# Kernel tuning notes

Hardware: AMD Instinct MI355X
Metric: run time of the kernel (lower is better)

Reference implementation:

```python
import jax, jax.numpy as jnp
import numpy as np

B, S, SK = 4, 256, 512
D, NH, NKV, HD = 1024, 16, 4, 64
DE, NE = 4096, 8
LANG_CODES = jnp.arange(4, 4 + NE)  # expert language codes (codes > 3 are routed)
LN_EPS = 1e-5


def setup_inputs() -> dict:
    key = jax.random.key(0)
    ks = jax.random.split(key, 32)
    sc = 0.02
    n = lambda k, shape: jax.random.normal(k, shape, jnp.float32)
    causal = jnp.where(jnp.tril(jnp.ones((S, S), bool)), 0.0, -1e9).astype(jnp.float32)
    inp = {
        "hidden_states": n(ks[0], (B, S, D)),
        "encoder_hidden_states": n(ks[1], (B, SK, D)),
        "attention_mask": jnp.broadcast_to(causal, (B, 1, S, S)),
        "encoder_attention_mask": jnp.zeros((B, 1, S, SK), jnp.float32),
        "langs": jax.random.randint(ks[2], (B, 2), 0, 12),
        "ln1_g": jnp.ones((D,), jnp.float32), "ln1_b": jnp.zeros((D,), jnp.float32),
        "sa_q_w": n(ks[3], (D, D)) * sc, "sa_q_b": jnp.zeros((D,), jnp.float32),
        "sa_k_w": n(ks[4], (D, NKV * HD)) * sc, "sa_k_b": jnp.zeros((NKV * HD,), jnp.float32),
        "sa_v_w": n(ks[5], (D, NKV * HD)) * sc, "sa_v_b": jnp.zeros((NKV * HD,), jnp.float32),
        "sa_o_w": n(ks[6], (D, D)) * sc, "sa_o_b": jnp.zeros((D,), jnp.float32),
        "ln2_g": jnp.ones((D,), jnp.float32), "ln2_b": jnp.zeros((D,), jnp.float32),
        "ca_q_w": n(ks[7], (D, D)) * sc, "ca_q_b": jnp.zeros((D,), jnp.float32),
        "ca_k_w": n(ks[8], (D, NKV * HD)) * sc, "ca_k_b": jnp.zeros((NKV * HD,), jnp.float32),
        "ca_v_w": n(ks[9], (D, NKV * HD)) * sc, "ca_v_b": jnp.zeros((NKV * HD,), jnp.float32),
        "ca_o_w": n(ks[10], (D, D)) * sc, "ca_o_b": jnp.zeros((D,), jnp.float32),
        "ln3_g": jnp.ones((D,), jnp.float32), "ln3_b": jnp.zeros((D,), jnp.float32),
        "moe_w1": n(ks[11], (NE, D, DE)) * sc,
        "moe_w2": n(ks[12], (NE, DE, D)) * sc,
        "moe_w3": n(ks[13], (NE, D, DE)) * sc,
    }
    return inp


def _ln(x, g, b):
    m = jnp.mean(x, -1, keepdims=True)
    v = jnp.var(x, -1, keepdims=True)
    return (x - m) * jax.lax.rsqrt(v + LN_EPS) * g + b


def _gqa(x, kv, qw, qb, kw, kb, vw, vb, ow, ob, mask):
    b, sq, _ = x.shape
    skv = kv.shape[1]
    q = ((x @ qw + qb) * HD ** -0.5).reshape(b, sq, NH, HD)
    k = (kv @ kw + kb).reshape(b, skv, NKV, HD)
    v = (kv @ vw + vb).reshape(b, skv, NKV, HD)
    rep = NH // NKV
    k = jnp.repeat(k, rep, axis=2)  # head h = kv_head*rep + r, matches repeat_kv
    v = jnp.repeat(v, rep, axis=2)
    scores = jnp.einsum('bqhd,bkhd->bhqk', q, k) + mask
    p = jax.nn.softmax(scores, axis=-1)
    o = jnp.einsum('bhqk,bkhd->bqhd', p, v).reshape(b, sq, NH * HD)
    return o @ ow + ob


def _moe(x, w1, w2, w3, langs):
    # routing: weight 1/(# lang codes > 3) per sequence; 1 if none
    counts = jnp.sum(langs > 3, axis=-1)
    rw = jnp.where(counts == 0, 1.0, 1.0 / jnp.maximum(counts, 1).astype(x.dtype))  # [B]
    match = jnp.any(langs[None, :, :] == LANG_CODES[:, None, None], axis=-1)  # [E,B]
    coef = match.astype(x.dtype) * rw[None, :]  # [E,B]
    h = jax.nn.gelu(jnp.einsum('bsd,edf->ebsf', x, w1), approximate=False) \
        * jnp.einsum('bsd,edf->ebsf', x, w3)
    out = jnp.einsum('ebsf,efd->ebsd', h, w2)
    return jnp.einsum('ebsd,eb->bsd', out, coef)


def reference(hidden_states, encoder_hidden_states, attention_mask, encoder_attention_mask,
              langs, ln1_g, ln1_b, sa_q_w, sa_q_b, sa_k_w, sa_k_b, sa_v_w, sa_v_b,
              sa_o_w, sa_o_b, ln2_g, ln2_b, ca_q_w, ca_q_b, ca_k_w, ca_k_b, ca_v_w,
              ca_v_b, ca_o_w, ca_o_b, ln3_g, ln3_b, moe_w1, moe_w2, moe_w3):
    # self attention (causal GQA, prefill, pre-LN)
    r = hidden_states
    h = _ln(hidden_states, ln1_g, ln1_b)
    h = _gqa(h, h, sa_q_w, sa_q_b, sa_k_w, sa_k_b, sa_v_w, sa_v_b, sa_o_w, sa_o_b,
             attention_mask)
    h = r + h
    # cross attention over encoder states
    r = h
    h = _ln(h, ln2_g, ln2_b)
    h = _gqa(h, encoder_hidden_states, ca_q_w, ca_q_b, ca_k_w, ca_k_b, ca_v_w, ca_v_b,
             ca_o_w, ca_o_b, encoder_attention_mask)
    h = r + h
    # language-routed MoE FFN
    r = h
    h = _ln(h, ln3_g, ln3_b)
    h = _moe(h, moe_w1, moe_w2, moe_w3, langs)
    return r + h
```

## Files before the change

### kernel.cpp

```cpp
#include <hip/hip_runtime.h>
#include <math.h>

#define B_   4
#define S_   256
#define SK_  512
#define D_   1024
#define NH_  16
#define NKV_ 4
#define HD_  64
#define DE_  4096
#define NE_  8

typedef __attribute__((ext_vector_type(8))) short bf16x8;
typedef __attribute__((ext_vector_type(4))) float f32x4;

__device__ __forceinline__ unsigned short f2b(float f) {
  union { float f; unsigned u; } v; v.f = f;
  unsigned r = v.u + 0x7FFF + ((v.u >> 16) & 1);
  return (unsigned short)(r >> 16);
}


__device__ __forceinline__ void stage_A_f32(const float* __restrict__ A, int lda, int k0, short* As) {
  int tid = threadIdx.x;
  int am = tid >> 2, ak8 = (tid & 3) * 8;
  const float* ap = A + (size_t)am * lda + k0 + ak8;
  float4 a0 = *(const float4*)ap;
  float4 a1 = *(const float4*)(ap + 4);
  const float* f0 = (const float*)&a0;
  const float* f1 = (const float*)&a1;
  bf16x8 v;
  v[0]=f2b(f0[0]); v[1]=f2b(f0[1]); v[2]=f2b(f0[2]); v[3]=f2b(f0[3]);
  v[4]=f2b(f1[0]); v[5]=f2b(f1[1]); v[6]=f2b(f1[2]); v[7]=f2b(f1[3]);
  *(bf16x8*)(As + am * 40 + ak8) = v;
}

__device__ __forceinline__ void stage_A_bf16(const short* __restrict__ A, int lda, int k0, short* As) {
  int tid = threadIdx.x;
  int am = tid >> 2, ak8 = (tid & 3) * 8;
  *(bf16x8*)(As + am * 40 + ak8) = *(const bf16x8*)(A + (size_t)am * lda + k0 + ak8);
}

__device__ __forceinline__ void stage_W_f32(const float* __restrict__ W, int ldw, int k0, short* Ws) {
  int tid = threadIdx.x;
  int wk2 = (tid & 15) * 2, wn4 = (tid >> 4) * 4;
  const float* wp = W + (size_t)(k0 + wk2) * ldw + wn4;
  float4 w0 = *(const float4*)wp;
  float4 w1 = *(const float4*)(wp + ldw);
  const float* f0 = (const float*)&w0;
  const float* f1 = (const float*)&w1;
#pragma unroll
  for (int c = 0; c < 4; ++c) {
    unsigned p = (unsigned)f2b(f0[c]) | ((unsigned)f2b(f1[c]) << 16);
    *(unsigned*)(Ws + (wn4 + c) * 40 + wk2) = p;
  }
}

__device__ __forceinline__ void mfma_quad(const short* As, const short* Ws, f32x4 acc[2][2]) {
  int lane = threadIdx.x & 63, wv = threadIdx.x >> 6;
  int wm = (wv & 1) * 32, wn = (wv >> 1) * 32;
  int quad = lane >> 4, l16 = lane & 15;
  bf16x8 a0 = *(const bf16x8*)(As + (wm + l16) * 40 + quad * 8);
  bf16x8 a1 = *(const bf16x8*)(As + (wm + 16 + l16) * 40 + quad * 8);
  bf16x8 b0 = *(const bf16x8*)(Ws + (wn + l16) * 40 + quad * 8);
  bf16x8 b1 = *(const bf16x8*)(Ws + (wn + 16 + l16) * 40 + quad * 8);
  acc[0][0] = __builtin_amdgcn_mfma_f32_16x16x32_bf16(a0, b0, acc[0][0], 0, 0, 0);
  acc[0][1] = __builtin_amdgcn_mfma_f32_16x16x32_bf16(a0, b1, acc[0][1], 0, 0, 0);
  acc[1][0] = __builtin_amdgcn_mfma_f32_16x16x32_bf16(a1, b0, acc[1][0], 0, 0, 0);
  acc[1][1] = __builtin_amdgcn_mfma_f32_16x16x32_bf16(a1, b1, acc[1][1], 0, 0, 0);
}

__device__ __forceinline__ void gemm_body(const float* A, const float* W, const float* bias,
                                          const float* resid, float* C, float scale,
                                          int N, int K, int bm, int bn,
                                          short* As, short* Ws) {
  f32x4 z4 = {0.f, 0.f, 0.f, 0.f};
  f32x4 acc[2][2] = {{z4, z4}, {z4, z4}};
  const float* Ab = A + (size_t)bm * K;
  const float* Wb = W + bn;
  for (int k0 = 0; k0 < K; k0 += 32) {
    stage_A_f32(Ab, K, k0, As);
    stage_W_f32(Wb, N, k0, Ws);
    __syncthreads();
    mfma_quad(As, Ws, acc);
    __syncthreads();
  }
  int lane = threadIdx.x & 63, wv = threadIdx.x >> 6;
  int wm = (wv & 1) * 32, wn = (wv >> 1) * 32;
  int quad = lane >> 4, l16 = lane & 15;
#pragma unroll
  for (int i = 0; i < 2; ++i)
#pragma unroll
    for (int j = 0; j < 2; ++j)
#pragma unroll
      for (int r = 0; r < 4; ++r) {
        int m = bm + wm + i * 16 + quad * 4 + r;
        int n = bn + wn + j * 16 + l16;
        float v = (acc[i][j][r] + bias[n]) * scale;
        if (resid) v += resid[(size_t)m * N + n];
        C[(size_t)m * N + n] = v;
      }
}

__global__ __launch_bounds__(256) void qkv_mfma(const float* __restrict__ xq, const float* __restrict__ xkv,
                                                const float* qw, const float* qb,
                                                const float* kw, const float* kb,
                                                const float* vw, const float* vb,
                                                float* qo, float* ko, float* vo,
                                                int Mq, int Mkv) {
  int z = blockIdx.z;
  const float *A, *W, *bias; float* out; int M, N; float scale;
  if (z == 0)      { A = xq;  W = qw; bias = qb; out = qo; M = Mq;  N = D_;  scale = 0.125f; }
  else if (z == 1) { A = xkv; W = kw; bias = kb; out = ko; M = Mkv; N = 256; scale = 1.0f; }
  else             { A = xkv; W = vw; bias = vb; out = vo; M = Mkv; N = 256; scale = 1.0f; }
  int bn = blockIdx.x * 64, bm = blockIdx.y * 64;
  if (bm >= M || bn >= N) return;
  __shared__ short As[64 * 40], Ws[64 * 40];
  gemm_body(A, W, bias, nullptr, out, scale, N, D_, bm, bn, As, Ws);
}

__global__ __launch_bounds__(256) void gemm_mfma(const float* __restrict__ A, const float* __restrict__ W,
                                                 const float* __restrict__ bias,
                                                 const float* resid, float* C,
                                                 float scale, int N, int K) {
  int bn = blockIdx.x * 64, bm = blockIdx.y * 64;
  __shared__ short As[64 * 40], Ws[64 * 40];
  gemm_body(A, W, bias, resid, C, scale, N, K, bm, bn, As, Ws);
}

__global__ __launch_bounds__(256) void moe_gate_mfma(const float* __restrict__ xln,
                                                     const float* __restrict__ W1,
                                                     const float* __restrict__ W3,
                                                     short* __restrict__ Hs,
                                                     const float* __restrict__ coef,
                                                     const int* __restrict__ slot) {
  int e = blockIdx.z;
  int bn = blockIdx.x * 64, bm = blockIdx.y * 64;
  int b = bm >> 8;
  if (coef[e * B_ + b] == 0.0f) return;
  int sl = slot[e * B_ + b];
  __shared__ short As[64 * 40], W1s[64 * 40], W3s[64 * 40];
  f32x4 z4 = {0.f, 0.f, 0.f, 0.f};
  f32x4 acc1[2][2] = {{z4, z4}, {z4, z4}};
  f32x4 acc3[2][2] = {{z4, z4}, {z4, z4}};
  const float* Ab  = xln + (size_t)bm * D_;
  const float* W1b = W1 + (size_t)e * D_ * DE_ + bn;
  const float* W3b = W3 + (size_t)e * D_ * DE_ + bn;
  for (int k0 = 0; k0 < D_; k0 += 32) {
    stage_A_f32(Ab, D_, k0, As);
    stage_W_f32(W1b, DE_, k0, W1s);
    stage_W_f32(W3b, DE_, k0, W3s);
    __syncthreads();
    mfma_quad(As, W1s, acc1);
    mfma_quad(As, W3s, acc3);
    __syncthreads();
  }
  int lane = threadIdx.x & 63, wv = threadIdx.x >> 6;
  int wm = (wv & 1) * 32, wn = (wv >> 1) * 32;
  int quad = lane >> 4, l16 = lane & 15;
  int rb = bm & 255;
  short* Hp = Hs + ((size_t)(sl * B_ + b) * S_ + rb) * DE_;
#pragma unroll
  for (int i = 0; i < 2; ++i)
#pragma unroll
    for (int j = 0; j < 2; ++j)
#pragma unroll
      for (int r = 0; r < 4; ++r) {
        int lm = wm + i * 16 + quad * 4 + r;
        int n  = bn + wn + j * 16 + l16;
        float c1 = acc1[i][j][r], c3 = acc3[i][j][r];
        float g = 0.5f * c1 * (1.0f + erff(c1 * 0.70710678118654752f));
        Hp[(size_t)lm * DE_ + n] = (short)f2b(g * c3);
      }
}

__global__ __launch_bounds__(256) void moe_down_mfma(const short* __restrict__ Hs,
                                                     const float* __restrict__ W2,
                                                     float* resid,
                                                     const float* __restrict__ coef,
                                                     const int* __restrict__ slot) {
  int z = blockIdx.z;
  int e = z >> 2, kc = z & 3;
  int bn = blockIdx.x * 64, bm = blockIdx.y * 64;
  int b = bm >> 8;
  float cf = coef[e * B_ + b];
  if (cf == 0.0f) return;
  int sl = slot[e * B_ + b];
  int rb = bm & 255;
  __shared__ short As[64 * 40], Ws[64 * 40];
  f32x4 z4 = {0.f, 0.f, 0.f, 0.f};
  f32x4 acc[2][2] = {{z4, z4}, {z4, z4}};
  const short* Ab = Hs + ((size_t)(sl * B_ + b) * S_ + rb) * DE_ + kc * 1024;
  const float* Wb = W2 + (size_t)e * DE_ * D_ + (size_t)kc * 1024 * D_ + bn;
  for (int k0 = 0; k0 < 1024; k0 += 32) {
    stage_A_bf16(Ab, DE_, k0, As);
    stage_W_f32(Wb, D_, k0, Ws);
    __syncthreads();
    mfma_quad(As, Ws, acc);
    __syncthreads();
  }
  int lane = threadIdx.x & 63, wv = threadIdx.x >> 6;
  int wm = (wv & 1) * 32, wn = (wv >> 1) * 32;
  int quad = lane >> 4, l16 = lane & 15;
#pragma unroll
  for (int i = 0; i < 2; ++i)
#pragma unroll
    for (int j = 0; j < 2; ++j)
#pragma unroll
      for (int r = 0; r < 4; ++r) {
        int m = bm + wm + i * 16 + quad * 4 + r;
        int n = bn + wn + j * 16 + l16;
        atomicAdd(&resid[(size_t)m * D_ + n], cf * acc[i][j][r]);
      }
}

__global__ __launch_bounds__(256) void ln_kernel(const float* __restrict__ x,
                                                 const float* __restrict__ g,
                                                 const float* __restrict__ be,
                                                 float* __restrict__ y) {
  int row = blockIdx.x, tid = threadIdx.x;
  const float4 v = ((const float4*)(x + (size_t)row * D_))[tid];
  float s  = v.x + v.y + v.z + v.w;
  float s2 = v.x*v.x + v.y*v.y + v.z*v.z + v.w*v.w;
  __shared__ float r1[256], r2[256];
  r1[tid] = s; r2[tid] = s2; __syncthreads();
  for (int off = 128; off > 0; off >>= 1) {
    if (tid < off) { r1[tid] += r1[tid+off]; r2[tid] += r2[tid+off]; }
    __syncthreads();
  }
  float mean = r1[0] * (1.0f / D_);
  float var  = r2[0] * (1.0f / D_) - mean * mean;
  float inv  = rsqrtf(var + 1e-5f);
  float* yr = y + (size_t)row * D_;
  int c = tid * 4;
  yr[c]   = (v.x - mean) * inv * g[c]   + be[c];
  yr[c+1] = (v.y - mean) * inv * g[c+1] + be[c+1];
  yr[c+2] = (v.z - mean) * inv * g[c+2] + be[c+2];
  yr[c+3] = (v.w - mean) * inv * g[c+3] + be[c+3];
}

__global__ __launch_bounds__(256) void qk_kernel(const float* __restrict__ qb,
                                                 const float* __restrict__ kb,
                                                 const float* __restrict__ mask,
                                                 float* __restrict__ sc,
                                                 int b0, int SKV) {
  int z = blockIdx.z;
  int zb = z >> 4, h = z & 15;
  int b = b0 + zb;
  int kvh = h >> 2;
  int bq = blockIdx.y * 64, bk = blockIdx.x * 64;
  __shared__ float As[16][64];
  __shared__ float Bs[16][64];
  int tid = threadIdx.x;
  int tx = tid & 15, ty = tid >> 4;
  int ar = tid >> 2, ac4 = (tid & 3) * 4;
  float acc[4][4] = {};
  for (int k0 = 0; k0 < HD_; k0 += 16) {
    float4 av = *(const float4*)(qb + (size_t)(b*S_ + bq + ar) * D_ + h*HD_ + k0 + ac4);
    As[ac4+0][ar] = av.x; As[ac4+1][ar] = av.y; As[ac4+2][ar] = av.z; As[ac4+3][ar] = av.w;
    float4 bv = *(const float4*)(kb + (size_t)(b*SKV + bk + ar) * (NKV_*HD_) + kvh*HD_ + k0 + ac4);
    Bs[ac4+0][ar] = bv.x; Bs[ac4+1][ar] = bv.y; Bs[ac4+2][ar] = bv.z; Bs[ac4+3][ar] = bv.w;
    __syncthreads();
#pragma unroll
    for (int kk = 0; kk < 16; ++kk) {
      float a0[4], w0[4];
#pragma unroll
      for (int i = 0; i < 4; ++i) a0[i] = As[kk][ty*4 + i];
#pragma unroll
      for (int j = 0; j < 4; ++j) w0[j] = Bs[kk][tx*4 + j];
#pragma unroll
      for (int i = 0; i < 4; ++i)
#pragma unroll
        for (int j = 0; j < 4; ++j) acc[i][j] += a0[i] * w0[j];
    }
    __syncthreads();
  }
#pragma unroll
  for (int i = 0; i < 4; ++i) {
    int qi = bq + ty*4 + i;
#pragma unroll
    for (int j = 0; j < 4; ++j) {
      int kc = bk + tx*4 + j;
      sc[((size_t)(zb*NH_ + h) * S_ + qi) * SKV + kc] =
          acc[i][j] + mask[((size_t)(b*S_ + qi)) * SKV + kc];
    }
  }
}

__global__ __launch_bounds__(256) void softmax_kernel(float* __restrict__ sc, int SKV, int nrows) {
  int row = blockIdx.x * 4 + (threadIdx.x >> 6);
  int lane = threadIdx.x & 63;
  if (row >= nrows) return;
  float* rp = sc + (size_t)row * SKV;
  float4 v[2];
  int nc = SKV >> 8;
  float mx = -1e30f;
#pragma unroll
  for (int c = 0; c < 2; ++c) {
    if (c < nc) {
      v[c] = *(float4*)(rp + c*256 + lane*4);
      mx = fmaxf(mx, fmaxf(fmaxf(v[c].x, v[c].y), fmaxf(v[c].z, v[c].w)));
    }
  }
#pragma unroll
  for (int m = 32; m > 0; m >>= 1) mx = fmaxf(mx, __shfl_xor(mx, m, 64));
  float ls = 0.f;
#pragma unroll
  for (int c = 0; c < 2; ++c) {
    if (c < nc) {
      v[c].x = __expf(v[c].x - mx); v[c].y = __expf(v[c].y - mx);
      v[c].z = __expf(v[c].z - mx); v[c].w = __expf(v[c].w - mx);
      ls += v[c].x + v[c].y + v[c].z + v[c].w;
    }
  }
#pragma unroll
  for (int m = 32; m > 0; m >>= 1) ls += __shfl_xor(ls, m, 64);
  float inv = 1.0f / ls;
#pragma unroll
  for (int c = 0; c < 2; ++c) {
    if (c < nc) {
      v[c].x *= inv; v[c].y *= inv; v[c].z *= inv; v[c].w *= inv;
      *(float4*)(rp + c*256 + lane*4) = v[c];
    }
  }
}

__global__ __launch_bounds__(256) void pv_kernel(const float* __restrict__ sc,
                                                 const float* __restrict__ vb,
                                                 float* __restrict__ ob,
                                                 int b0, int SKV) {
  int z = blockIdx.y;
  int zb = z >> 4, h = z & 15;
  int b = b0 + zb;
  int kvh = h >> 2;
  int bq = blockIdx.x * 64;
  __shared__ float As[16][64];
  __shared__ float Bs[16][64];
  int tid = threadIdx.x;
  int tx = tid & 15, ty = tid >> 4;
  int ar = tid >> 2, ac4 = (tid & 3) * 4;
  int wr = tid >> 4, wc = (tid & 15) * 4;
  float acc[4][4] = {};
  for (int k0 = 0; k0 < SKV; k0 += 16) {
    float4 av = *(const float4*)(sc + ((size_t)(zb*NH_ + h) * S_ + bq + ar) * SKV + k0 + ac4);
    As[ac4+0][ar] = av.x; As[ac4+1][ar] = av.y; As[ac4+2][ar] = av.z; As[ac4+3][ar] = av.w;
    float4 bv = *(const float4*)(vb + (size_t)(b*SKV + k0 + wr) * (NKV_*HD_) + kvh*HD_ + wc);
    Bs[wr][wc+0] = bv.x; Bs[wr][wc+1] = bv.y;
    Bs[wr][wc+2] = bv.z; Bs[wr][wc+3] = bv.w;
    __syncthreads();
#pragma unroll
    for (int kk = 0; kk < 16; ++kk) {
      float a0[4], w0[4];
#pragma unroll
      for (int i = 0; i < 4; ++i) a0[i] = As[kk][ty*4 + i];
#pragma unroll
      for (int j = 0; j < 4; ++j) w0[j] = Bs[kk][tx*4 + j];
#pragma unroll
      for (int i = 0; i < 4; ++i)
#pragma unroll
        for (int j = 0; j < 4; ++j) acc[i][j] += a0[i] * w0[j];
    }
    __syncthreads();
  }
#pragma unroll
  for (int i = 0; i < 4; ++i) {
    int qi = bq + ty*4 + i;
#pragma unroll
    for (int j = 0; j < 4; ++j) {
      int d = tx*4 + j;
      ob[(size_t)(b*S_ + qi) * D_ + h*HD_ + d] = acc[i][j];
    }
  }
}

__global__ void coef_kernel(const int* __restrict__ langs, float* __restrict__ coef,
                            int* __restrict__ slot) {
  int t = threadIdx.x;
  if (t < NE_ * B_) {
    int e = t >> 2, b = t & 3;
    int l0 = langs[b*2], l1 = langs[b*2 + 1];
    int counts = (l0 > 3) + (l1 > 3);
    float rw = (counts == 0) ? 1.0f : 1.0f / (float)counts;
    bool m = (l0 == 4 + e) || (l1 == 4 + e);
    coef[t] = m ? rw : 0.0f;
    int s = 0;
    for (int ep = 0; ep < e; ++ep) s += ((l0 == 4 + ep) || (l1 == 4 + ep)) ? 1 : 0;
    slot[t] = s;
// ... 24 lines not shown
  const float* caqb = (const float*)d_in[18];
  const float* cakw = (const float*)d_in[19];
  const float* cakb = (const float*)d_in[20];
  const float* cavw = (const float*)d_in[21];
  const float* cavb = (const float*)d_in[22];
  const float* caow = (const float*)d_in[23];
  const float* caob = (const float*)d_in[24];
  const float* ln3g = (const float*)d_in[25];
  const float* ln3b = (const float*)d_in[26];
  const float* w1   = (const float*)d_in[27];
  const float* w2   = (const float*)d_in[28];
  const float* w3   = (const float*)d_in[29];

  float* resid = (float*)d_out;

  float* ws = (float*)d_ws;
  float* xln   = ws;  ws += B_*S_*D_;
  float* qbuf  = ws;  ws += B_*S_*D_;
  float* kbuf  = ws;  ws += B_*SK_*NKV_*HD_;
  float* vbuf  = ws;  ws += B_*SK_*NKV_*HD_;
  float* abuf  = ws;  ws += B_*S_*D_;
  float* Hreg  = ws;  ws += B_*S_*DE_;
  float* coef  = ws;  ws += 32;
  int*   slot  = (int*)ws; ws += 32;
  float* scb   = Hreg;
  short* Hs    = (short*)Hreg;

  dim3 blk(256);
  const int M = B_ * S_;

  ln_kernel<<<M, blk, 0, stream>>>(hidden, ln1g, ln1b, xln);
  qkv_mfma<<<dim3(16, 16, 3), blk, 0, stream>>>(xln, xln, saqw, saqb, sakw, sakb, savw, savb,
                                                qbuf, kbuf, vbuf, M, M);
  qk_kernel<<<dim3(S_/64, S_/64, 4*NH_), blk, 0, stream>>>(qbuf, kbuf, amask, scb, 0, S_);
  softmax_kernel<<<(4*NH_*S_)/4, blk, 0, stream>>>(scb, S_, 4*NH_*S_);
  pv_kernel<<<dim3(S_/64, 4*NH_), blk, 0, stream>>>(scb, vbuf, abuf, 0, S_);
  gemm_mfma<<<dim3(16, 16), blk, 0, stream>>>(abuf, saow, saob, hidden, resid, 1.0f, D_, D_);

  ln_kernel<<<M, blk, 0, stream>>>(resid, ln2g, ln2b, xln);
  qkv_mfma<<<dim3(16, 32, 3), blk, 0, stream>>>(xln, enc, caqw, caqb, cakw, cakb, cavw, cavb,
                                                qbuf, kbuf, vbuf, M, B_*SK_);
  for (int b0 = 0; b0 < B_; b0 += 2) {
    qk_kernel<<<dim3(SK_/64, S_/64, 2*NH_), blk, 0, stream>>>(qbuf, kbuf, emask, scb, b0, SK_);
    softmax_kernel<<<(2*NH_*S_)/4, blk, 0, stream>>>(scb, SK_, 2*NH_*S_);
    pv_kernel<<<dim3(S_/64, 2*NH_), blk, 0, stream>>>(scb, vbuf, abuf, b0, SK_);
  }
  gemm_mfma<<<dim3(16, 16), blk, 0, stream>>>(abuf, caow, caob, resid, resid, 1.0f, D_, D_);

  ln_kernel<<<M, blk, 0, stream>>>(resid, ln3g, ln3b, xln);
  coef_kernel<<<1, 64, 0, stream>>>(langs, coef, slot);
  moe_gate_mfma<<<dim3(DE_/64, M/64, NE_), blk, 0, stream>>>(xln, w1, w3, Hs, coef, slot);
  moe_down_mfma<<<dim3(D_/64, M/64, NE_*4), blk, 0, stream>>>(Hs, w2, resid, coef, slot);
}
```

Measured before the change: 861.9 us.

## Rewrite attention path with bf16 activations and MFMA QK/PV kernels

Replaces the fp32 FMA attention score and PV kernels with MFMA bf16 kernels. LayerNorm outputs, Q/K/V projections and the attention output are now stored as bf16, and V is written transposed so PV can read contiguous fragments. Softmax writes bf16 probabilities in place. The projection GEMMs drop LDS staging and load fragments straight from global memory, converting the weights on the fly. This cuts memory traffic and moves the attention matmuls onto matrix cores, at the cost of bf16 rounding on intermediates and uncoalesced strided weight loads without LDS reuse.

```diff
diff --git a/kernel.cpp b/kernel.cpp
--- a/kernel.cpp
+++ b/kernel.cpp
@@ -14,121 +14,318 @@
 typedef __attribute__((ext_vector_type(8))) short bf16x8;
 typedef __attribute__((ext_vector_type(4))) float f32x4;
 
+struct __align__(8) s4 { short x, y, z, w; };
+
+#define MFMA(a,b,c) __builtin_amdgcn_mfma_f32_16x16x32_bf16(a,b,c,0,0,0)
+
 __device__ __forceinline__ unsigned short f2b(float f) {
   union { float f; unsigned u; } v; v.f = f;
   unsigned r = v.u + 0x7FFF + ((v.u >> 16) & 1);
   return (unsigned short)(r >> 16);
 }
 
-
-__device__ __forceinline__ void stage_A_f32(const float* __restrict__ A, int lda, int k0, short* As) {
-  int tid = threadIdx.x;
-  int am = tid >> 2, ak8 = (tid & 3) * 8;
-  const float* ap = A + (size_t)am * lda + k0 + ak8;
-  float4 a0 = *(const float4*)ap;
-  float4 a1 = *(const float4*)(ap + 4);
-  const float* f0 = (const float*)&a0;
-  const float* f1 = (const float*)&a1;
-  bf16x8 v;
-  v[0]=f2b(f0[0]); v[1]=f2b(f0[1]); v[2]=f2b(f0[2]); v[3]=f2b(f0[3]);
-  v[4]=f2b(f1[0]); v[5]=f2b(f1[1]); v[6]=f2b(f1[2]); v[7]=f2b(f1[3]);
-  *(bf16x8*)(As + am * 40 + ak8) = v;
-}
-
-__device__ __forceinline__ void stage_A_bf16(const short* __restrict__ A, int lda, int k0, short* As) {
-  int tid = threadIdx.x;
-  int am = tid >> 2, ak8 = (tid & 3) * 8;
-  *(bf16x8*)(As + am * 40 + ak8) = *(const bf16x8*)(A + (size_t)am * lda + k0 + ak8);
-}
-
-__device__ __forceinline__ void stage_W_f32(const float* __restrict__ W, int ldw, int k0, short* Ws) {
-  int tid = threadIdx.x;
-  int wk2 = (tid & 15) * 2, wn4 = (tid >> 4) * 4;
-  const float* wp = W + (size_t)(k0 + wk2) * ldw + wn4;
-  float4 w0 = *(const float4*)wp;
-  float4 w1 = *(const float4*)(wp + ldw);
-  const float* f0 = (const float*)&w0;
-  const float* f1 = (const float*)&w1;
-#pragma unroll
-  for (int c = 0; c < 4; ++c) {
-    unsigned p = (unsigned)f2b(f0[c]) | ((unsigned)f2b(f1[c]) << 16);
-    *(unsigned*)(Ws + (wn4 + c) * 40 + wk2) = p;
-  }
-}
-
-__device__ __forceinline__ void mfma_quad(const short* As, const short* Ws, f32x4 acc[2][2]) {
-  int lane = threadIdx.x & 63, wv = threadIdx.x >> 6;
-  int wm = (wv & 1) * 32, wn = (wv >> 1) * 32;
-  int quad = lane >> 4, l16 = lane & 15;
-  bf16x8 a0 = *(const bf16x8*)(As + (wm + l16) * 40 + quad * 8);
-  bf16x8 a1 = *(const bf16x8*)(As + (wm + 16 + l16) * 40 + quad * 8);
-  bf16x8 b0 = *(const bf16x8*)(Ws + (wn + l16) * 40 + quad * 8);
-  bf16x8 b1 = *(const bf16x8*)(Ws + (wn + 16 + l16) * 40 + quad * 8);
-  acc[0][0] = __builtin_amdgcn_mfma_f32_16x16x32_bf16(a0, b0, acc[0][0], 0, 0, 0);
-  acc[0][1] = __builtin_amdgcn_mfma_f32_16x16x32_bf16(a0, b1, acc[0][1], 0, 0, 0);
-  acc[1][0] = __builtin_amdgcn_mfma_f32_16x16x32_bf16(a1, b0, acc[1][0], 0, 0, 0);
-  acc[1][1] = __builtin_amdgcn_mfma_f32_16x16x32_bf16(a1, b1, acc[1][1], 0, 0, 0);
-}
-
-__device__ __forceinline__ void gemm_body(const float* A, const float* W, const float* bias,
-                                          const float* resid, float* C, float scale,
-                                          int N, int K, int bm, int bn,
-                                          short* As, short* Ws) {
-  f32x4 z4 = {0.f, 0.f, 0.f, 0.f};
-  f32x4 acc[2][2] = {{z4, z4}, {z4, z4}};
-  const float* Ab = A + (size_t)bm * K;
-  const float* Wb = W + bn;
-  for (int k0 = 0; k0 < K; k0 += 32) {
-    stage_A_f32(Ab, K, k0, As);
-    stage_W_f32(Wb, N, k0, Ws);
+__device__ __forceinline__ bf16x8 load_w_frag(const float* __restrict__ wp, int ldw) {
+  union { unsigned u[4]; bf16x8 v; } r;
+#pragma unroll
+  for (int j = 0; j < 4; ++j) {
+    unsigned u0 = __float_as_uint(wp[(size_t)(2*j)   * ldw]) + 0x8000u;
+    unsigned u1 = __float_as_uint(wp[(size_t)(2*j+1) * ldw]) + 0x8000u;
+    r.u[j] = (u0 >> 16) | (u1 & 0xffff0000u);
+  }
+  return r.v;
+}
+
+__global__ __launch_bounds__(256) void ln_kernel(const float* __restrict__ x,
+                                                 const float* __restrict__ g,
+                                                 const float* __restrict__ be,
+                                                 short* __restrict__ y) {
+  int row = blockIdx.x, tid = threadIdx.x;
+  const float4 v = ((const float4*)(x + (size_t)row * D_))[tid];
+  float s  = v.x + v.y + v.z + v.w;
+  float s2 = v.x*v.x + v.y*v.y + v.z*v.z + v.w*v.w;
+  __shared__ float r1[256], r2[256];
+  r1[tid] = s; r2[tid] = s2; __syncthreads();
+  for (int off = 128; off > 0; off >>= 1) {
+    if (tid < off) { r1[tid] += r1[tid+off]; r2[tid] += r2[tid+off]; }
     __syncthreads();
-    mfma_quad(As, Ws, acc);
-    __syncthreads();
-  }
-  int lane = threadIdx.x & 63, wv = threadIdx.x >> 6;
-  int wm = (wv & 1) * 32, wn = (wv >> 1) * 32;
-  int quad = lane >> 4, l16 = lane & 15;
-#pragma unroll
-  for (int i = 0; i < 2; ++i)
-#pragma unroll
-    for (int j = 0; j < 2; ++j)
-#pragma unroll
-      for (int r = 0; r < 4; ++r) {
-        int m = bm + wm + i * 16 + quad * 4 + r;
-        int n = bn + wn + j * 16 + l16;
-        float v = (acc[i][j][r] + bias[n]) * scale;
-        if (resid) v += resid[(size_t)m * N + n];
-        C[(size_t)m * N + n] = v;
-      }
-}
-
-__global__ __launch_bounds__(256) void qkv_mfma(const float* __restrict__ xq, const float* __restrict__ xkv,
-                                                const float* qw, const float* qb,
-                                                const float* kw, const float* kb,
-                                                const float* vw, const float* vb,
-                                                float* qo, float* ko, float* vo,
-                                                int Mq, int Mkv) {
-  int z = blockIdx.z;
-  const float *A, *W, *bias; float* out; int M, N; float scale;
-  if (z == 0)      { A = xq;  W = qw; bias = qb; out = qo; M = Mq;  N = D_;  scale = 0.125f; }
-  else if (z == 1) { A = xkv; W = kw; bias = kb; out = ko; M = Mkv; N = 256; scale = 1.0f; }
-  else             { A = xkv; W = vw; bias = vb; out = vo; M = Mkv; N = 256; scale = 1.0f; }
-  int bn = blockIdx.x * 64, bm = blockIdx.y * 64;
-  if (bm >= M || bn >= N) return;
-  __shared__ short As[64 * 40], Ws[64 * 40];
-  gemm_body(A, W, bias, nullptr, out, scale, N, D_, bm, bn, As, Ws);
-}
-
-__global__ __launch_bounds__(256) void gemm_mfma(const float* __restrict__ A, const float* __restrict__ W,
+  }
+  float mean = r1[0] * (1.0f / D_);
+  float var  = r2[0] * (1.0f / D_) - mean * mean;
+  float inv  = rsqrtf(var + 1e-5f);
+  int c = tid * 4;
+  s4 o;
+  o.x = (short)f2b((v.x - mean) * inv * g[c]   + be[c]);
+  o.y = (short)f2b((v.y - mean) * inv * g[c+1] + be[c+1]);
+  o.z = (short)f2b((v.z - mean) * inv * g[c+2] + be[c+2]);
+  o.w = (short)f2b((v.w - mean) * inv * g[c+3] + be[c+3]);
+  *(s4*)(y + (size_t)row * D_ + c) = o;
+}
+
+__global__ void cast_f2b(const float* __restrict__ in, short* __restrict__ out, int n) {
+  int i = (blockIdx.x * 256 + threadIdx.x) * 4;
+  if (i < n) {
+    float4 v = *(const float4*)(in + i);
+    s4 o; o.x=(short)f2b(v.x); o.y=(short)f2b(v.y); o.z=(short)f2b(v.z); o.w=(short)f2b(v.w);
+    *(s4*)(out + i) = o;
+  }
+}
+
+__global__ __launch_bounds__(256) void proj_mfma(const short* __restrict__ A,
+                                                 const float* __restrict__ W,
                                                  const float* __restrict__ bias,
-                                                 const float* resid, float* C,
+                                                 short* __restrict__ Cb,
                                                  float scale, int N, int K) {
   int bn = blockIdx.x * 64, bm = blockIdx.y * 64;
-  __shared__ short As[64 * 40], Ws[64 * 40];
-  gemm_body(A, W, bias, resid, C, scale, N, K, bm, bn, As, Ws);
-}
-
-__global__ __launch_bounds__(256) void moe_gate_mfma(const float* __restrict__ xln,
+  int lane = threadIdx.x & 63, wv = threadIdx.x >> 6;
+  int wm = (wv & 1) * 32, wn = (wv >> 1) * 32;
+  int quad = lane >> 4, l16 = lane & 15;
+  f32x4 z4 = {0.f,0.f,0.f,0.f};
+  f32x4 acc[2][2] = {{z4,z4},{z4,z4}};
+  const short* a0p = A + (size_t)(bm + wm + l16) * K;
+  const short* a1p = a0p + (size_t)16 * K;
+  const float* w0p = W + bn + wn + l16;
+  const float* w1p = w0p + 16;
+#pragma unroll 2
+  for (int k0 = 0; k0 < K; k0 += 32) {
+    int ka = k0 + quad * 8;
+    bf16x8 a0 = *(const bf16x8*)(a0p + ka);
+    bf16x8 a1 = *(const bf16x8*)(a1p + ka);
+    bf16x8 b0 = load_w_frag(w0p + (size_t)ka * N, N);
+    bf16x8 b1 = load_w_frag(w1p + (size_t)ka * N, N);
+    acc[0][0] = MFMA(a0, b0, acc[0][0]);
+    acc[0][1] = MFMA(a0, b1, acc[0][1]);
+    acc[1][0] = MFMA(a1, b0, acc[1][0]);
+    acc[1][1] = MFMA(a1, b1, acc[1][1]);
+  }
+#pragma unroll
+  for (int i = 0; i < 2; ++i)
+#pragma unroll
+    for (int j = 0; j < 2; ++j) {
+      int n = bn + wn + j*16 + l16;
+      float bs = bias[n];
+#pragma unroll
+      for (int r = 0; r < 4; ++r) {
+        int m = bm + wm + i*16 + quad*4 + r;
+        Cb[(size_t)m * N + n] = (short)f2b((acc[i][j][r] + bs) * scale);
+      }
+    }
+}
+
+__global__ __launch_bounds__(256) void proj_v_mfma(const short* __restrict__ A,
+                                                   const float* __restrict__ W,
+                                                   const float* __restrict__ bias,
+                                                   short* __restrict__ vT,
+                                                   int SKV, int K) {
+  const int N = 256;
+  int bn = blockIdx.x * 64, bm = blockIdx.y * 64;
+  int lane = threadIdx.x & 63, wv = threadIdx.x >> 6;
+  int wm = (wv & 1) * 32, wn = (wv >> 1) * 32;
+  int quad = lane >> 4, l16 = lane & 15;
+  f32x4 z4 = {0.f,0.f,0.f,0.f};
+  f32x4 acc[2][2] = {{z4,z4},{z4,z4}};
+  const short* a0p = A + (size_t)(bm + wm + l16) * K;
+  const short* a1p = a0p + (size_t)16 * K;
+  const float* w0p = W + bn + wn + l16;
+  const float* w1p = w0p + 16;
+#pragma unroll 2
+  for (int k0 = 0; k0 < K; k0 += 32) {
+    int ka = k0 + quad * 8;
+    bf16x8 a0 = *(const bf16x8*)(a0p + ka);
+    bf16x8 a1 = *(const bf16x8*)(a1p + ka);
+    bf16x8 b0 = load_w_frag(w0p + (size_t)ka * N, N);
+    bf16x8 b1 = load_w_frag(w1p + (size_t)ka * N, N);
+    acc[0][0] = MFMA(a0, b0, acc[0][0]);
+    acc[0][1] = MFMA(a0, b1, acc[0][1]);
+    acc[1][0] = MFMA(a1, b0, acc[1][0]);
+    acc[1][1] = MFMA(a1, b1, acc[1][1]);
+  }
+  __shared__ float T[64][65];
+#pragma unroll
+  for (int i = 0; i < 2; ++i)
+#pragma unroll
+    for (int j = 0; j < 2; ++j) {
+      int nl = wn + j*16 + l16;
+      float bs = bias[bn + nl];
+#pragma unroll
+      for (int r = 0; r < 4; ++r)
+        T[nl][wm + i*16 + quad*4 + r] = acc[i][j][r] + bs;
+    }
+  __syncthreads();
+  int t = threadIdx.x;
+  int nl = t >> 2, m4 = (t & 3) * 16;
+  int bb = bm / SKV, skv0 = bm % SKV;
+  short* dst = vT + ((size_t)bb * 256 + bn + nl) * 512 + skv0 + m4;
+  bf16x8 o0, o1;
+#pragma unroll
+  for (int ii = 0; ii < 8; ++ii) o0[ii] = (short)f2b(T[nl][m4 + ii]);
+#pragma unroll
+  for (int ii = 0; ii < 8; ++ii) o1[ii] = (short)f2b(T[nl][m4 + 8 + ii]);
+  *(bf16x8*)dst = o0;
+  *(bf16x8*)(dst + 8) = o1;
+}
+
+__global__ __launch_bounds__(256) void proj_o_mfma(const short* __restrict__ A,
+                                                   const float* __restrict__ W,
+                                                   const float* __restrict__ bias,
+                                                   const float* __restrict__ rin,
+                                                   float* __restrict__ C, int N, int K) {
+  int bn = blockIdx.x * 64, bm = blockIdx.y * 64;
+  int lane = threadIdx.x & 63, wv = threadIdx.x >> 6;
+  int wm = (wv & 1) * 32, wn = (wv >> 1) * 32;
+  int quad = lane >> 4, l16 = lane & 15;
+  f32x4 z4 = {0.f,0.f,0.f,0.f};
+  f32x4 acc[2][2] = {{z4,z4},{z4,z4}};
+  const short* a0p = A + (size_t)(bm + wm + l16) * K;
+  const short* a1p = a0p + (size_t)16 * K;
+  const float* w0p = W + bn + wn + l16;
+  const float* w1p = w0p + 16;
+#pragma unroll 2
+  for (int k0 = 0; k0 < K; k0 += 32) {
+    int ka = k0 + quad * 8;
+    bf16x8 a0 = *(const bf16x8*)(a0p + ka);
+    bf16x8 a1 = *(const bf16x8*)(a1p + ka);
+    bf16x8 b0 = load_w_frag(w0p + (size_t)ka * N, N);
+    bf16x8 b1 = load_w_frag(w1p + (size_t)ka * N, N);
+    acc[0][0] = MFMA(a0, b0, acc[0][0]);
+    acc[0][1] = MFMA(a0, b1, acc[0][1]);
+    acc[1][0] = MFMA(a1, b0, acc[1][0]);
+    acc[1][1] = MFMA(a1, b1, acc[1][1]);
+  }
+#pragma unroll
+  for (int i = 0; i < 2; ++i)
+#pragma unroll
+    for (int j = 0; j < 2; ++j) {
+      int n = bn + wn + j*16 + l16;
+      float bs = bias[n];
+#pragma unroll
+      for (int r = 0; r < 4; ++r) {
+        int m = bm + wm + i*16 + quad*4 + r;
+        C[(size_t)m * N + n] = acc[i][j][r] + bs + rin[(size_t)m * N + n];
+      }
+    }
+}
+
+__global__ __launch_bounds__(256) void qk_mfma(const short* __restrict__ Q,
+                                               const short* __restrict__ Kb,
+                                               const float* __restrict__ mask,
+                                               float* __restrict__ sc,
+                                               int b0, int SKV) {
+  int z = blockIdx.z, zb = z >> 4, h = z & 15, b = b0 + zb, kvh = h >> 2;
+  int bk = blockIdx.x * 64, bq = blockIdx.y * 64;
+  int lane = threadIdx.x & 63, wv = threadIdx.x >> 6;
+  int wm = (wv & 1) * 32, wn = (wv >> 1) * 32;
+  int quad = lane >> 4, l16 = lane & 15;
+  f32x4 z4 = {0.f,0.f,0.f,0.f};
+  f32x4 acc[2][2] = {{z4,z4},{z4,z4}};
+  const short* q0 = Q + (size_t)(b*S_ + bq + wm + l16) * D_ + h * HD_;
+  const short* q1 = q0 + (size_t)16 * D_;
+  const short* k0p = Kb + (size_t)(b*SKV + bk + wn + l16) * (NKV_*HD_) + kvh * HD_;
+  const short* k1p = k0p + (size_t)16 * (NKV_*HD_);
+#pragma unroll
+  for (int d0 = 0; d0 < HD_; d0 += 32) {
+    int ka = d0 + quad * 8;
+    bf16x8 a0 = *(const bf16x8*)(q0 + ka);
+    bf16x8 a1 = *(const bf16x8*)(q1 + ka);
+    bf16x8 b0f = *(const bf16x8*)(k0p + ka);
+    bf16x8 b1f = *(const bf16x8*)(k1p + ka);
+    acc[0][0] = MFMA(a0, b0f, acc[0][0]);
+    acc[0][1] = MFMA(a0, b1f, acc[0][1]);
+    acc[1][0] = MFMA(a1, b0f, acc[1][0]);
+    acc[1][1] = MFMA(a1, b1f, acc[1][1]);
+  }
+#pragma unroll
+  for (int i = 0; i < 2; ++i)
+#pragma unroll
+    for (int j = 0; j < 2; ++j) {
+      int n = bk + wn + j*16 + l16;
+#pragma unroll
+      for (int r = 0; r < 4; ++r) {
+        int m = bq + wm + i*16 + quad*4 + r;
+        sc[((size_t)(zb*NH_ + h) * S_ + m) * SKV + n] =
+            acc[i][j][r] + mask[((size_t)(b*S_ + m)) * SKV + n];
+      }
+    }
+}
+
+__global__ __launch_bounds__(256) void softmax_kernel(float* __restrict__ sc, int SKV, int nrows) {
+  int row = blockIdx.x * 4 + (threadIdx.x >> 6);
+  int lane = threadIdx.x & 63;
+  if (row >= nrows) return;
+  float* rp = sc + (size_t)row * SKV;
+  short* sp = (short*)rp;
+  float4 v[2];
+  int nc = SKV >> 8;
+  float mx = -1e30f;
+#pragma unroll
+  for (int c = 0; c < 2; ++c)
+    if (c < nc) {
+      v[c] = *(float4*)(rp + c*256 + lane*4);
+      mx = fmaxf(mx, fmaxf(fmaxf(v[c].x, v[c].y), fmaxf(v[c].z, v[c].w)));
+    }
+#pragma unroll
+  for (int m = 32; m > 0; m >>= 1) mx = fmaxf(mx, __shfl_xor(mx, m, 64));
+  float ls = 0.f;
+#pragma unroll
+  for (int c = 0; c < 2; ++c)
+    if (c < nc) {
+      v[c].x = __expf(v[c].x - mx); v[c].y = __expf(v[c].y - mx);
+      v[c].z = __expf(v[c].z - mx); v[c].w = __expf(v[c].w - mx);
+      ls += v[c].x + v[c].y + v[c].z + v[c].w;
+    }
+#pragma unroll
+  for (int m = 32; m > 0; m >>= 1) ls += __shfl_xor(ls, m, 64);
+  float inv = 1.0f / ls;
+#pragma unroll
+  for (int c = 0; c < 2; ++c)
+    if (c < nc) {
+      s4 o;
+      o.x = (short)f2b(v[c].x * inv); o.y = (short)f2b(v[c].y * inv);
+      o.z = (short)f2b(v[c].z * inv); o.w = (short)f2b(v[c].w * inv);
+      *(s4*)(sp + c*256 + lane*4) = o;
+    }
+}
+
+__global__ __launch_bounds__(256) void pv_mfma(const short* __restrict__ Pb,
+                                               const short* __restrict__ vT,
+                                               short* __restrict__ ob,
+                                               int b0, int SKV) {
+  int z = blockIdx.y, zb = z >> 4, h = z & 15, b = b0 + zb, kvh = h >> 2;
+  int bq = blockIdx.x * 64;
+  int lane = threadIdx.x & 63, wv = threadIdx.x >> 6;
+  int wm = (wv & 1) * 32, wn = (wv >> 1) * 32;
+  int quad = lane >> 4, l16 = lane & 15;
+  f32x4 z4 = {0.f,0.f,0.f,0.f};
+  f32x4 acc[2][2] = {{z4,z4},{z4,z4}};
+  const short* p0 = Pb + ((size_t)(zb*NH_ + h) * S_ + bq + wm + l16) * (size_t)(2*SKV);
+  const short* p1 = p0 + (size_t)16 * 2 * SKV;
+  const short* v0 = vT + ((size_t)b * 256 + kvh*64 + wn + l16) * 512;
+  const short* v1 = v0 + (size_t)16 * 512;
+#pragma unroll 4
+  for (int k0 = 0; k0 < SKV; k0 += 32) {
+    int ka = k0 + quad * 8;
+    bf16x8 a0 = *(const bf16x8*)(p0 + ka);
+    bf16x8 a1 = *(const bf16x8*)(p1 + ka);
+    bf16x8 b0f = *(const bf16x8*)(v0 + ka);
+    bf16x8 b1f = *(const bf16x8*)(v1 + ka);
+    acc[0][0] = MFMA(a0, b0f, acc[0][0]);
+    acc[0][1] = MFMA(a0, b1f, acc[0][1]);
+    acc[1][0] = MFMA(a1, b0f, acc[1][0]);
+    acc[1][1] = MFMA(a1, b1f, acc[1][1]);
+  }
+#pragma unroll
+  for (int i = 0; i < 2; ++i)
+#pragma unroll
+    for (int j = 0; j < 2; ++j) {
+      int n = wn + j*16 + l16;
+#pragma unroll
+      for (int r = 0; r < 4; ++r) {
+        int m = bq + wm + i*16 + quad*4 + r;
+        ob[(size_t)(b*S_ + m) * D_ + h*HD_ + n] = (short)f2b(acc[i][j][r]);
+      }
+    }
+}
+
+__global__ __launch_bounds__(256) void moe_gate_mfma(const short* __restrict__ xlnb,
                                                      const float* __restrict__ W1,
                                                      const float* __restrict__ W3,
                                                      short* __restrict__ Hs,
@@ -139,39 +336,50 @@
   int b = bm >> 8;
   if (coef[e * B_ + b] == 0.0f) return;
   int sl = slot[e * B_ + b];
-  __shared__ short As[64 * 40], W1s[64 * 40], W3s[64 * 40];
-  f32x4 z4 = {0.f, 0.f, 0.f, 0.f};
-  f32x4 acc1[2][2] = {{z4, z4}, {z4, z4}};
-  f32x4 acc3[2][2] = {{z4, z4}, {z4, z4}};
-  const float* Ab  = xln + (size_t)bm * D_;
-  const float* W1b = W1 + (size_t)e * D_ * DE_ + bn;
-  const float* W3b = W3 + (size_t)e * D_ * DE_ + bn;
+  int lane = threadIdx.x & 63, wv = threadIdx.x >> 6;
+  int wm = (wv & 1) * 32, wn = (wv >> 1) * 32;
+  int quad = lane >> 4, l16 = lane & 15;
+  f32x4 z4 = {0.f,0.f,0.f,0.f};
+  f32x4 acc1[2][2] = {{z4,z4},{z4,z4}};
+  f32x4 acc3[2][2] = {{z4,z4},{z4,z4}};
+  const short* a0p = xlnb + (size_t)(bm + wm + l16) * D_;
+  const short* a1p = a0p + (size_t)16 * D_;
+  const float* w1p0 = W1 + (size_t)e * D_ * DE_ + bn + wn + l16;
+  const float* w1p1 = w1p0 + 16;
+  const float* w3p0 = W3 + (size_t)e * D_ * DE_ + bn + wn + l16;
+  const float* w3p1 = w3p0 + 16;
+#pragma unroll 2
   for (int k0 = 0; k0 < D_; k0 += 32) {
-    stage_A_f32(Ab, D_, k0, As);
-    stage_W_f32(W1b, DE_, k0, W1s);
-    stage_W_f32(W3b, DE_, k0, W3s);
-    __syncthreads();
-    mfma_quad(As, W1s, acc1);
-    mfma_quad(As, W3s, acc3);
-    __syncthreads();
-  }
-  int lane = threadIdx.x & 63, wv = threadIdx.x >> 6;
-  int wm = (wv & 1) * 32, wn = (wv >> 1) * 32;
-  int quad = lane >> 4, l16 = lane & 15;
-  int rb = bm & 255;
-  short* Hp = Hs + ((size_t)(sl * B_ + b) * S_ + rb) * DE_;
-#pragma unroll
-  for (int i = 0; i < 2; ++i)
-#pragma unroll
-    for (int j = 0; j < 2; ++j)
+    int ka = k0 + quad * 8;
+    bf16x8 a0 = *(const bf16x8*)(a0p + ka);
+    bf16x8 a1 = *(const bf16x8*)(a1p + ka);
+    bf16x8 b10 = load_w_frag(w1p0 + (size_t)ka * DE_, DE_);
+    bf16x8 b11 = load_w_frag(w1p1 + (size_t)ka * DE_, DE_);
+    bf16x8 b30 = load_w_frag(w3p0 + (size_t)ka * DE_, DE_);
+    bf16x8 b31 = load_w_frag(w3p1 + (size_t)ka * DE_, DE_);
+    acc1[0][0] = MFMA(a0, b10, acc1[0][0]);
+    acc1[0][1] = MFMA(a0, b11, acc1[0][1]);
+    acc1[1][0] = MFMA(a1, b10, acc1[1][0]);
+    acc1[1][1] = MFMA(a1, b11, acc1[1][1]);
+    acc3[0][0] = MFMA(a0, b30, acc3[0][0]);
+    acc3[0][1] = MFMA(a0, b31, acc3[0][1]);
+    acc3[1][0] = MFMA(a1, b30, acc3[1][0]);
+    acc3[1][1] = MFMA(a1, b31, acc3[1][1]);
+  }
+  short* Hp = Hs + ((size_t)(sl * B_ + b) * S_ + (bm & 255)) * DE_;
+#pragma unroll
+  for (int i = 0; i < 2; ++i)
+#pragma unroll
+    for (int j = 0; j < 2; ++j) {
+      int n = bn + wn + j*16 + l16;
 #pragma unroll
       for (int r = 0; r < 4; ++r) {
-        int lm = wm + i * 16 + quad * 4 + r;
-        int n  = bn + wn + j * 16 + l16;
+        int lm = wm + i*16 + quad*4 + r;
         float c1 = acc1[i][j][r], c3 = acc3[i][j][r];
         float g = 0.5f * c1 * (1.0f + erff(c1 * 0.70710678118654752f));
         Hp[(size_t)lm * DE_ + n] = (short)f2b(g * c3);
       }
+    }
 }
 
 __global__ __launch_bounds__(256) void moe_down_mfma(const short* __restrict__ Hs,
@@ -179,198 +387,45 @@
                                                      float* resid,
                                                      const float* __restrict__ coef,
                                                      const int* __restrict__ slot) {
-  int z = blockIdx.z;
-  int e = z >> 2, kc = z & 3;
+  int zc = blockIdx.z;
+  int e = zc >> 2, kc = zc & 3;
   int bn = blockIdx.x * 64, bm = blockIdx.y * 64;
   int b = bm >> 8;
   float cf = coef[e * B_ + b];
   if (cf == 0.0f) return;
   int sl = slot[e * B_ + b];
-  int rb = bm & 255;
-  __shared__ short As[64 * 40], Ws[64 * 40];
-  f32x4 z4 = {0.f, 0.f, 0.f, 0.f};
-  f32x4 acc[2][2] = {{z4, z4}, {z4, z4}};
-  const short* Ab = Hs + ((size_t)(sl * B_ + b) * S_ + rb) * DE_ + kc * 1024;
-  const float* Wb = W2 + (size_t)e * DE_ * D_ + (size_t)kc * 1024 * D_ + bn;
+  int lane = threadIdx.x & 63, wv = threadIdx.x >> 6;
+  int wm = (wv & 1) * 32, wn = (wv >> 1) * 32;
+  int quad = lane >> 4, l16 = lane & 15;
+  f32x4 z4 = {0.f,0.f,0.f,0.f};
+  f32x4 acc[2][2] = {{z4,z4},{z4,z4}};
+  const short* a0p = Hs + ((size_t)(sl * B_ + b) * S_ + (bm & 255) + wm + l16) * DE_ + kc * 1024;
+  const short* a1p = a0p + (size_t)16 * DE_;
+  const float* w0p = W2 + (size_t)e * DE_ * D_ + (size_t)kc * 1024 * D_ + bn + wn + l16;
+  const float* w1p = w0p + 16;
+#pragma unroll 2
   for (int k0 = 0; k0 < 1024; k0 += 32) {
-    stage_A_bf16(Ab, DE_, k0, As);
-    stage_W_f32(Wb, D_, k0, Ws);
-    __syncthreads();
-    mfma_quad(As, Ws, acc);
-    __syncthreads();
-  }
-  int lane = threadIdx.x & 63, wv = threadIdx.x >> 6;
-  int wm = (wv & 1) * 32, wn = (wv >> 1) * 32;
-  int quad = lane >> 4, l16 = lane & 15;
-#pragma unroll
-  for (int i = 0; i < 2; ++i)
-#pragma unroll
-    for (int j = 0; j < 2; ++j)
+    int ka = k0 + quad * 8;
+    bf16x8 a0 = *(const bf16x8*)(a0p + ka);
+    bf16x8 a1 = *(const bf16x8*)(a1p + ka);
+    bf16x8 b0 = load_w_frag(w0p + (size_t)ka * D_, D_);
+    bf16x8 b1 = load_w_frag(w1p + (size_t)ka * D_, D_);
+    acc[0][0] = MFMA(a0, b0, acc[0][0]);
+    acc[0][1] = MFMA(a0, b1, acc[0][1]);
+    acc[1][0] = MFMA(a1, b0, acc[1][0]);
+    acc[1][1] = MFMA(a1, b1, acc[1][1]);
+  }
+#pragma unroll
+  for (int i = 0; i < 2; ++i)
+#pragma unroll
+    for (int j = 0; j < 2; ++j) {
+      int n = bn + wn + j*16 + l16;
 #pragma unroll
       for (int r = 0; r < 4; ++r) {
-        int m = bm + wm + i * 16 + quad * 4 + r;
-        int n = bn + wn + j * 16 + l16;
+        int m = bm + wm + i*16 + quad*4 + r;
         atomicAdd(&resid[(size_t)m * D_ + n], cf * acc[i][j][r]);
       }
-}
-
-__global__ __launch_bounds__(256) void ln_kernel(const float* __restrict__ x,
-                                                 const float* __restrict__ g,
-                                                 const float* __restrict__ be,
-                                                 float* __restrict__ y) {
-  int row = blockIdx.x, tid = threadIdx.x;
-  const float4 v = ((const float4*)(x + (size_t)row * D_))[tid];
-  float s  = v.x + v.y + v.z + v.w;
-  float s2 = v.x*v.x + v.y*v.y + v.z*v.z + v.w*v.w;
-  __shared__ float r1[256], r2[256];
-  r1[tid] = s; r2[tid] = s2; __syncthreads();
-  for (int off = 128; off > 0; off >>= 1) {
-    if (tid < off) { r1[tid] += r1[tid+off]; r2[tid] += r2[tid+off]; }
-    __syncthreads();
-  }
-  float mean = r1[0] * (1.0f / D_);
-  float var  = r2[0] * (1.0f / D_) - mean * mean;
-  float inv  = rsqrtf(var + 1e-5f);
-  float* yr = y + (size_t)row * D_;
-  int c = tid * 4;
-  yr[c]   = (v.x - mean) * inv * g[c]   + be[c];
-  yr[c+1] = (v.y - mean) * inv * g[c+1] + be[c+1];
-  yr[c+2] = (v.z - mean) * inv * g[c+2] + be[c+2];
-  yr[c+3] = (v.w - mean) * inv * g[c+3] + be[c+3];
-}
-
-__global__ __launch_bounds__(256) void qk_kernel(const float* __restrict__ qb,
-                                                 const float* __restrict__ kb,
-                                                 const float* __restrict__ mask,
-                                                 float* __restrict__ sc,
-                                                 int b0, int SKV) {
-  int z = blockIdx.z;
-  int zb = z >> 4, h = z & 15;
-  int b = b0 + zb;
-  int kvh = h >> 2;
-  int bq = blockIdx.y * 64, bk = blockIdx.x * 64;
-  __shared__ float As[16][64];
-  __shared__ float Bs[16][64];
-  int tid = threadIdx.x;
-  int tx = tid & 15, ty = tid >> 4;
-  int ar = tid >> 2, ac4 = (tid & 3) * 4;
-  float acc[4][4] = {};
-  for (int k0 = 0; k0 < HD_; k0 += 16) {
-    float4 av = *(const float4*)(qb + (size_t)(b*S_ + bq + ar) * D_ + h*HD_ + k0 + ac4);
-    As[ac4+0][ar] = av.x; As[ac4+1][ar] = av.y; As[ac4+2][ar] = av.z; As[ac4+3][ar] = av.w;
-    float4 bv = *(const float4*)(kb + (size_t)(b*SKV + bk + ar) * (NKV_*HD_) + kvh*HD_ + k0 + ac4);
-    Bs[ac4+0][ar] = bv.x; Bs[ac4+1][ar] = bv.y; Bs[ac4+2][ar] = bv.z; Bs[ac4+3][ar] = bv.w;
-    __syncthreads();
-#pragma unroll
-    for (int kk = 0; kk < 16; ++kk) {
-      float a0[4], w0[4];
-#pragma unroll
-      for (int i = 0; i < 4; ++i) a0[i] = As[kk][ty*4 + i];
-#pragma unroll
-      for (int j = 0; j < 4; ++j) w0[j] = Bs[kk][tx*4 + j];
-#pragma unroll
-      for (int i = 0; i < 4; ++i)
-#pragma unroll
-        for (int j = 0; j < 4; ++j) acc[i][j] += a0[i] * w0[j];
-    }
-    __syncthreads();
-  }
-#pragma unroll
-  for (int i = 0; i < 4; ++i) {
-    int qi = bq + ty*4 + i;
-#pragma unroll
-    for (int j = 0; j < 4; ++j) {
-      int kc = bk + tx*4 + j;
-      sc[((size_t)(zb*NH_ + h) * S_ + qi) * SKV + kc] =
-          acc[i][j] + mask[((size_t)(b*S_ + qi)) * SKV + kc];
-    }
-  }
-}
-
-__global__ __launch_bounds__(256) void softmax_kernel(float* __restrict__ sc, int SKV, int nrows) {
-  int row = blockIdx.x * 4 + (threadIdx.x >> 6);
-  int lane = threadIdx.x & 63;
-  if (row >= nrows) return;
-  float* rp = sc + (size_t)row * SKV;
-  float4 v[2];
-  int nc = SKV >> 8;
-  float mx = -1e30f;
-#pragma unroll
-  for (int c = 0; c < 2; ++c) {
-    if (c < nc) {
-      v[c] = *(float4*)(rp + c*256 + lane*4);
-      mx = fmaxf(mx, fmaxf(fmaxf(v[c].x, v[c].y), fmaxf(v[c].z, v[c].w)));
-    }
-  }
-#pragma unroll
-  for (int m = 32; m > 0; m >>= 1) mx = fmaxf(mx, __shfl_xor(mx, m, 64));
-  float ls = 0.f;
-#pragma unroll
-  for (int c = 0; c < 2; ++c) {
-    if (c < nc) {
-      v[c].x = __expf(v[c].x - mx); v[c].y = __expf(v[c].y - mx);
-      v[c].z = __expf(v[c].z - mx); v[c].w = __expf(v[c].w - mx);
-      ls += v[c].x + v[c].y + v[c].z + v[c].w;
-    }
-  }
-#pragma unroll
-  for (int m = 32; m > 0; m >>= 1) ls += __shfl_xor(ls, m, 64);
-  float inv = 1.0f / ls;
-#pragma unroll
-  for (int c = 0; c < 2; ++c) {
-    if (c < nc) {
-      v[c].x *= inv; v[c].y *= inv; v[c].z *= inv; v[c].w *= inv;
-      *(float4*)(rp + c*256 + lane*4) = v[c];
-    }
-  }
-}
-
-__global__ __launch_bounds__(256) void pv_kernel(const float* __restrict__ sc,
-                                                 const float* __restrict__ vb,
-                                                 float* __restrict__ ob,
-                                                 int b0, int SKV) {
-  int z = blockIdx.y;
-  int zb = z >> 4, h = z & 15;
-  int b = b0 + zb;
-  int kvh = h >> 2;
-  int bq = blockIdx.x * 64;
-  __shared__ float As[16][64];
-  __shared__ float Bs[16][64];
-  int tid = threadIdx.x;
-  int tx = tid & 15, ty = tid >> 4;
-  int ar = tid >> 2, ac4 = (tid & 3) * 4;
-  int wr = tid >> 4, wc = (tid & 15) * 4;
-  float acc[4][4] = {};
-  for (int k0 = 0; k0 < SKV; k0 += 16) {
-    float4 av = *(const float4*)(sc + ((size_t)(zb*NH_ + h) * S_ + bq + ar) * SKV + k0 + ac4);
-    As[ac4+0][ar] = av.x; As[ac4+1][ar] = av.y; As[ac4+2][ar] = av.z; As[ac4+3][ar] = av.w;
-    float4 bv = *(const float4*)(vb + (size_t)(b*SKV + k0 + wr) * (NKV_*HD_) + kvh*HD_ + wc);
-    Bs[wr][wc+0] = bv.x; Bs[wr][wc+1] = bv.y;
-    Bs[wr][wc+2] = bv.z; Bs[wr][wc+3] = bv.w;
-    __syncthreads();
-#pragma unroll
-    for (int kk = 0; kk < 16; ++kk) {
-      float a0[4], w0[4];
-#pragma unroll
-      for (int i = 0; i < 4; ++i) a0[i] = As[kk][ty*4 + i];
-#pragma unroll
-      for (int j = 0; j < 4; ++j) w0[j] = Bs[kk][tx*4 + j];
-#pragma unroll
-      for (int i = 0; i < 4; ++i)
-#pragma unroll
-        for (int j = 0; j < 4; ++j) acc[i][j] += a0[i] * w0[j];
-    }
-    __syncthreads();
-  }
-#pragma unroll
-  for (int i = 0; i < 4; ++i) {
-    int qi = bq + ty*4 + i;
-#pragma unroll
-    for (int j = 0; j < 4; ++j) {
-      int d = tx*4 + j;
-      ob[(size_t)(b*S_ + qi) * D_ + h*HD_ + d] = acc[i][j];
-    }
-  }
+    }
 }
 
 __global__ void coef_kernel(const int* __restrict__ langs, float* __restrict__ coef,
@@ -425,41 +480,44 @@
 
   float* resid = (float*)d_out;
 
+  const int M = B_ * S_;
   float* ws = (float*)d_ws;
-  float* xln   = ws;  ws += B_*S_*D_;
-  float* qbuf  = ws;  ws += B_*S_*D_;
-  float* kbuf  = ws;  ws += B_*SK_*NKV_*HD_;
-  float* vbuf  = ws;  ws += B_*SK_*NKV_*HD_;
-  float* abuf  = ws;  ws += B_*S_*D_;
-  float* Hreg  = ws;  ws += B_*S_*DE_;
-  float* coef  = ws;  ws += 32;
-  int*   slot  = (int*)ws; ws += 32;
-  float* scb   = Hreg;
-  short* Hs    = (short*)Hreg;
+  short* xlnb = (short*)ws;  ws += (M * D_) / 2;
+  short* encb = (short*)ws;  ws += (B_ * SK_ * D_) / 2;
+  short* qb   = (short*)ws;  ws += (M * D_) / 2;
+  short* kb   = (short*)ws;  ws += (B_ * SK_ * 256) / 2;
+  short* vT   = (short*)ws;  ws += (B_ * 256 * 512) / 2;
+  short* ab   = (short*)ws;  ws += (M * D_) / 2;
+  float* scb  = ws;          ws += B_ * NH_ * S_ * S_;
+  float* coef = ws;          ws += 32;
+  int*   slot = (int*)ws;    ws += 32;
+  short* Hs   = (short*)scb;
 
   dim3 blk(256);
-  const int M = B_ * S_;
-
-  ln_kernel<<<M, blk, 0, stream>>>(hidden, ln1g, ln1b, xln);
-  qkv_mfma<<<dim3(16, 16, 3), blk, 0, stream>>>(xln, xln, saqw, saqb, sakw, sakb, savw, savb,
-                                                qbuf, kbuf, vbuf, M, M);
-  qk_kernel<<<dim3(S_/64, S_/64, 4*NH_), blk, 0, stream>>>(qbuf, kbuf, amask, scb, 0, S_);
+
+  ln_kernel<<<M, blk, 0, stream>>>(hidden, ln1g, ln1b, xlnb);
+  proj_mfma<<<dim3(16, 16), blk, 0, stream>>>(xlnb, saqw, saqb, qb, 0.125f, D_, D_);
+  proj_mfma<<<dim3(4, 16), blk, 0, stream>>>(xlnb, sakw, sakb, kb, 1.0f, 256, D_);
+  proj_v_mfma<<<dim3(4, 16), blk, 0, stream>>>(xlnb, savw, savb, vT, 256, D_);
+  qk_mfma<<<dim3(4, 4, 4*NH_), blk, 0, stream>>>(qb, kb, amask, scb, 0, S_);
   softmax_kernel<<<(4*NH_*S_)/4, blk, 0, stream>>>(scb, S_, 4*NH_*S_);
-  pv_kernel<<<dim3(S_/64, 4*NH_), blk, 0, stream>>>(scb, vbuf, abuf, 0, S_);
-  gemm_mfma<<<dim3(16, 16), blk, 0, stream>>>(abuf, saow, saob, hidden, resid, 1.0f, D_, D_);
-
-  ln_kernel<<<M, blk, 0, stream>>>(resid, ln2g, ln2b, xln);
-  qkv_mfma<<<dim3(16, 32, 3), blk, 0, stream>>>(xln, enc, caqw, caqb, cakw, cakb, cavw, cavb,
-                                                qbuf, kbuf, vbuf, M, B_*SK_);
+  pv_mfma<<<dim3(4, 4*NH_), blk, 0, stream>>>((short*)scb, vT, ab, 0, S_);
+  proj_o_mfma<<<dim3(16, 16), blk, 0, stream>>>(ab, saow, saob, hidden, resid, D_, D_);
+
+  ln_kernel<<<M, blk, 0, stream>>>(resid, ln2g, ln2b, xlnb);
+  proj_mfma<<<dim3(16, 16), blk, 0, stream>>>(xlnb, caqw, caqb, qb, 0.125f, D_, D_);
+  cast_f2b<<<(B_*SK_*D_)/1024, blk, 0, stream>>>(enc, encb, B_*SK_*D_);
+  proj_mfma<<<dim3(4, 32), blk, 0, stream>>>(encb, cakw, cakb, kb, 1.0f, 256, D_);
+  proj_v_mfma<<<dim3(4, 32), blk, 0, stream>>>(encb, cavw, cavb, vT, 512, D_);
   for (int b0 = 0; b0 < B_; b0 += 2) {
-    qk_kernel<<<dim3(SK_/64, S_/64, 2*NH_), blk, 0, stream>>>(qbuf, kbuf, emask, scb, b0, SK_);
+    qk_mfma<<<dim3(8, 4, 2*NH_), blk, 0, stream>>>(qb, kb, emask, scb, b0, SK_);
     softmax_kernel<<<(2*NH_*S_)/4, blk, 0, stream>>>(scb, SK_, 2*NH_*S_);
-    pv_kernel<<<dim3(S_/64, 2*NH_), blk, 0, stream>>>(scb, vbuf, abuf, b0, SK_);
-  }
-  gemm_mfma<<<dim3(16, 16), blk, 0, stream>>>(abuf, caow, caob, resid, resid, 1.0f, D_, D_);
-
-  ln_kernel<<<M, blk, 0, stream>>>(resid, ln3g, ln3b, xln);
+    pv_mfma<<<dim3(4, 2*NH_), blk, 0, stream>>>((short*)scb, vT, ab, b0, SK_);
+  }
+  proj_o_mfma<<<dim3(16, 16), blk, 0, stream>>>(ab, caow, caob, resid, resid, D_, D_);
+
+  ln_kernel<<<M, blk, 0, stream>>>(resid, ln3g, ln3b, xlnb);
   coef_kernel<<<1, 64, 0, stream>>>(langs, coef, slot);
-  moe_gate_mfma<<<dim3(DE_/64, M/64, NE_), blk, 0, stream>>>(xln, w1, w3, Hs, coef, slot);
+  moe_gate_mfma<<<dim3(DE_/64, M/64, NE_), blk, 0, stream>>>(xlnb, w1, w3, Hs, coef, slot);
   moe_down_mfma<<<dim3(D_/64, M/64, NE_*4), blk, 0, stream>>>(Hs, w2, resid, coef, slot);
 }
```

New measurement: 820.0 us. 1.05x faster.
